# Optimization experiments

Measured on AMD Instinct MI355X. Metric: run time of the kernel, lower is better.

## Reference

```python
import jax, jax.numpy as jnp
import numpy as np

D_MODEL = 2048
D_STATE = 16
KER = 4
DT_RANK = D_MODEL // 16  # mamba default: ceil(d_model/16) = 128
B_SZ = 2
SEQ = 1024


def setup_inputs() -> dict:
    key = jax.random.key(0)
    ks = jax.random.split(key, 8)
    s = 0.02
    return {
        "x": jax.random.normal(ks[0], (B_SZ, SEQ, D_MODEL), jnp.float32),
        # in_proj: d_model -> 2*d_inner (expand=1 so d_inner=d_model)
        "W_in": jax.random.normal(ks[1], (2 * D_MODEL, D_MODEL), jnp.float32) * s,
        # depthwise causal conv, one kernel of length KER per channel
        "conv_w": jax.random.normal(ks[2], (D_MODEL, KER), jnp.float32) * s,
        "conv_b": jnp.zeros((D_MODEL,), jnp.float32),
        # x_proj: d_inner -> dt_rank + 2*d_state
        "W_xproj": jax.random.normal(ks[3], (DT_RANK + 2 * D_STATE, D_MODEL), jnp.float32) * s,
        # dt_proj: dt_rank -> d_inner
        "W_dt": jax.random.normal(ks[4], (D_MODEL, DT_RANK), jnp.float32) * s,
        "b_dt": jax.random.uniform(ks[5], (D_MODEL,), jnp.float32, -4.0, -2.0),
        # S4D-real init: A = -[1..d_state] per channel, stored as log
        "A_log": jnp.log(jnp.broadcast_to(jnp.arange(1, D_STATE + 1, dtype=jnp.float32), (D_MODEL, D_STATE))),
        "Dskip": jnp.ones((D_MODEL,), jnp.float32),
        # out_proj: d_inner -> d_model
        "W_out": jax.random.normal(ks[6], (D_MODEL, D_MODEL), jnp.float32) * s,
    }


def _mamba(x, W_in, conv_w, conv_b, W_xproj, W_dt, b_dt, A_log, Dskip, W_out):
    Bsz, L, dm = x.shape
    d_state = A_log.shape[1]
    dt_rank = W_dt.shape[1]
    K = conv_w.shape[1]

    # in_proj -> gate z and ssm input u
    xz = x @ W_in.T                      # [B, L, 2*d_inner]
    u, z = jnp.split(xz, 2, axis=-1)     # each [B, L, d_inner]

    # causal depthwise conv1d over time, then SiLU
    up = jnp.pad(u, ((0, 0), (K - 1, 0), (0, 0)))
    conv = conv_b + sum(conv_w[:, k] * up[:, k:k + L, :] for k in range(K))
    u = jax.nn.silu(conv)                # [B, L, d_inner]

    # input-dependent dt, B, C
    x_dbl = u @ W_xproj.T                # [B, L, dt_rank + 2*d_state]
    dt_r = x_dbl[..., :dt_rank]
    Bm = x_dbl[..., dt_rank:dt_rank + d_state]      # [B, L, N]
    Cm = x_dbl[..., dt_rank + d_state:]             # [B, L, N]
    dt = jax.nn.softplus(dt_r @ W_dt.T + b_dt)      # [B, L, d_inner]

    A = -jnp.exp(A_log)                             # [d_inner, N]
    dA = jnp.exp(dt[..., None] * A)                 # [B, L, d_inner, N]
    dBu = dt[..., None] * Bm[:, :, None, :] * u[..., None]  # [B, L, d_inner, N]

    def step(h, inp):
        dA_t, dBu_t, C_t = inp
        h = dA_t * h + dBu_t                        # [B, d_inner, N]
        y_t = jnp.einsum('bdn,bn->bd', h, C_t)      # [B, d_inner]
        return h, y_t

    h0 = jnp.zeros((Bsz, dm, d_state), dtype=x.dtype)
    _, ys = jax.lax.scan(step, h0,
                         (dA.swapaxes(0, 1), dBu.swapaxes(0, 1), Cm.swapaxes(0, 1)))
    y = ys.swapaxes(0, 1) + u * Dskip               # [B, L, d_inner]
    y = y * jax.nn.silu(z)
    return y @ W_out.T                              # [B, L, d_model]


def reference(x, W_in, conv_w, conv_b, W_xproj, W_dt, b_dt, A_log, Dskip, W_out):
    return _mamba(x, W_in, conv_w, conv_b, W_xproj, W_dt, b_dt, A_log, Dskip, W_out)
```

## Files before the change

### kernel.cpp

```cpp
#include <hip/hip_runtime.h>
#include <hip/hip_bf16.h>


#define D_MODEL 2048
#define D_STATE 16
#define KER 4
#define DT_RANK 128
#define B_SZ 2
#define SEQ 1024
#define BL (B_SZ * SEQ)
#define XPROJ_N (DT_RANK + 2 * D_STATE)
#define NC 32
#define TC (SEQ / NC)

using f32x4  = __attribute__((ext_vector_type(4))) float;
using bf16x8 = __attribute__((ext_vector_type(8))) __bf16;
using bf16x4 = __attribute__((ext_vector_type(4))) __bf16;

__device__ __forceinline__ float softplusf(float x) {
    return (x > 20.f) ? x : log1pf(__expf(x));
}
__device__ __forceinline__ float siluf(float x) {
    return x / (1.f + __expf(-x));
}

__global__ __launch_bounds__(256) void split_kernel(
    const float* __restrict__ src,
    __bf16* __restrict__ hi, __bf16* __restrict__ lo, int n4)
{
    int i = blockIdx.x * 256 + threadIdx.x;
    if (i >= n4) return;
    float4 v = *reinterpret_cast<const float4*>(&src[(size_t)i * 4]);
    bf16x4 hv, lv;
    float f[4] = {v.x, v.y, v.z, v.w};
    #pragma unroll
    for (int j = 0; j < 4; ++j) {
        __bf16 h = (__bf16)f[j];
        hv[j] = h;
        lv[j] = (__bf16)(f[j] - (float)h);
    }
    *reinterpret_cast<bf16x4*>(&hi[(size_t)i * 4]) = hv;
    *reinterpret_cast<bf16x4*>(&lo[(size_t)i * 4]) = lv;
}

__global__ __launch_bounds__(256, 2) void gemm_bf3(
    const __bf16* __restrict__ Ah, const __bf16* __restrict__ Al,
    const __bf16* __restrict__ Wh, const __bf16* __restrict__ Wl,
    float* __restrict__ C, int N_, int K)
{
    __shared__ __align__(16) __bf16 lds[4 * 128 * 64];
    __bf16* sAh = lds;
    __bf16* sAl = lds + 8192;
    __bf16* sWh = lds + 16384;
    __bf16* sWl = lds + 24576;

    const int tid = threadIdx.x;
    const int bm = blockIdx.y * 128;
    const int bn = blockIdx.x * 128;
    const int w  = tid >> 6;
    const int l  = tid & 63;
    const int wr = (w >> 1) * 64;
    const int wc = (w & 1) * 64;
    const int fr = l & 15;
    const int fq = l >> 4;

    f32x4 acc[4][4] = {};

    for (int k0 = 0; k0 < K; k0 += 64) {
        #pragma unroll
        for (int i = 0; i < 4; ++i) {
            const int f  = i * 256 + tid;
            const int r  = f >> 3;
            const int ss = f & 7;
            const int gs = ss ^ (r & 7);
            const size_t ga = (size_t)(bm + r) * K + k0 + gs * 8;
            const size_t gw = (size_t)(bn + r) * K + k0 + gs * 8;
            __builtin_amdgcn_global_load_lds(
                (const __attribute__((address_space(1))) void*)(Ah + ga),
                (__attribute__((address_space(3))) void*)(sAh + (size_t)f * 8), 16, 0, 0);
            __builtin_amdgcn_global_load_lds(
                (const __attribute__((address_space(1))) void*)(Al + ga),
                (__attribute__((address_space(3))) void*)(sAl + (size_t)f * 8), 16, 0, 0);
            __builtin_amdgcn_global_load_lds(
                (const __attribute__((address_space(1))) void*)(Wh + gw),
                (__attribute__((address_space(3))) void*)(sWh + (size_t)f * 8), 16, 0, 0);
            __builtin_amdgcn_global_load_lds(
                (const __attribute__((address_space(1))) void*)(Wl + gw),
                (__attribute__((address_space(3))) void*)(sWl + (size_t)f * 8), 16, 0, 0);
        }
        __syncthreads();

        #pragma unroll
        for (int ks = 0; ks < 2; ++ks) {
            bf16x8 ah[4], al[4], wh[4], wl[4];
            #pragma unroll
            for (int t = 0; t < 4; ++t) {
                const int ra = wr + t * 16 + fr;
                const int sa = (ks * 4 + fq) ^ (ra & 7);
                ah[t] = *reinterpret_cast<const bf16x8*>(&sAh[ra * 64 + sa * 8]);
                al[t] = *reinterpret_cast<const bf16x8*>(&sAl[ra * 64 + sa * 8]);
                const int rw = wc + t * 16 + fr;
                const int sw = (ks * 4 + fq) ^ (rw & 7);
                wh[t] = *reinterpret_cast<const bf16x8*>(&sWh[rw * 64 + sw * 8]);
                wl[t] = *reinterpret_cast<const bf16x8*>(&sWl[rw * 64 + sw * 8]);
            }
            #pragma unroll
            for (int mt = 0; mt < 4; ++mt)
                #pragma unroll
                for (int nt = 0; nt < 4; ++nt) {
                    acc[mt][nt] = __builtin_amdgcn_mfma_f32_16x16x32_bf16(
                        ah[mt], wh[nt], acc[mt][nt], 0, 0, 0);
                    acc[mt][nt] = __builtin_amdgcn_mfma_f32_16x16x32_bf16(
                        ah[mt], wl[nt], acc[mt][nt], 0, 0, 0);
                    acc[mt][nt] = __builtin_amdgcn_mfma_f32_16x16x32_bf16(
                        al[mt], wh[nt], acc[mt][nt], 0, 0, 0);
                }
        }
        __syncthreads();
    }

    #pragma unroll
    for (int mt = 0; mt < 4; ++mt)
        #pragma unroll
        for (int nt = 0; nt < 4; ++nt)
            #pragma unroll
            for (int j = 0; j < 4; ++j)
                C[(size_t)(bm + wr + mt * 16 + fq * 4 + j) * N_
                  + bn + wc + nt * 16 + fr] = acc[mt][nt][j];
}

#define BM 64
#define BN 64
#define BKT 32

template <int EPI>
__global__ __launch_bounds__(256) void gemm_nt(
    const float* __restrict__ A, int lda,
    const float* __restrict__ W, int ldw,
    float* __restrict__ C, int ldc,
    const float* __restrict__ bias,
    int M, int N, int K)
{
    __shared__ float As[BKT][BM + 4];
    __shared__ float Ws[BKT][BN + 4];

    const int tid = threadIdx.x;
    const int bm = blockIdx.y * BM;
    const int bn = blockIdx.x * BN;
    const int tx = tid & 15;
    const int ty = tid >> 4;

    float acc[4][4] = {};

    for (int k0 = 0; k0 < K; k0 += BKT) {
        #pragma unroll
        for (int i = 0; i < 2; ++i) {
            int f = tid + i * 256;
            int row = f >> 3;
            int kq  = f & 7;
            float4 v = *reinterpret_cast<const float4*>(
                &A[(size_t)(bm + row) * lda + k0 + kq * 4]);
            As[kq * 4 + 0][row] = v.x;
            As[kq * 4 + 1][row] = v.y;
            As[kq * 4 + 2][row] = v.z;
            As[kq * 4 + 3][row] = v.w;
        }
        #pragma unroll
        for (int i = 0; i < 2; ++i) {
            int f = tid + i * 256;
            int row = f >> 3;
            int kq  = f & 7;
            int gn = bn + row;
            float4 v = make_float4(0.f, 0.f, 0.f, 0.f);
            if (gn < N) {
                v = *reinterpret_cast<const float4*>(
                    &W[(size_t)gn * ldw + k0 + kq * 4]);
            }
            Ws[kq * 4 + 0][row] = v.x;
            Ws[kq * 4 + 1][row] = v.y;
            Ws[kq * 4 + 2][row] = v.z;
            Ws[kq * 4 + 3][row] = v.w;
        }
        __syncthreads();

        #pragma unroll
        for (int kk = 0; kk < BKT; ++kk) {
            float4 a4 = *reinterpret_cast<const float4*>(&As[kk][ty * 4]);
            float4 w4 = *reinterpret_cast<const float4*>(&Ws[kk][tx * 4]);
            float a[4] = {a4.x, a4.y, a4.z, a4.w};
            float wv[4] = {w4.x, w4.y, w4.z, w4.w};
            #pragma unroll
            for (int i = 0; i < 4; ++i)
                #pragma unroll
                for (int j = 0; j < 4; ++j)
                    acc[i][j] = fmaf(a[i], wv[j], acc[i][j]);
        }
        __syncthreads();
    }

    #pragma unroll
    for (int i = 0; i < 4; ++i) {
        int gm = bm + ty * 4 + i;
        #pragma unroll
        for (int j = 0; j < 4; ++j) {
            int gn = bn + tx * 4 + j;
            if (gn < N) {
                float v = acc[i][j];
                if (EPI == 1) v = softplusf(v + bias[gn]);
                C[(size_t)gm * ldc + gn] = v;
            }
        }
    }
}

#define XBM 64
#define XBN 32
#define XKS 8
#define XKC (D_MODEL / XKS)

__global__ __launch_bounds__(256) void xdbl_partial(
    const float* __restrict__ A,
    const float* __restrict__ W,
    float* __restrict__ P)
{
    __shared__ float As[BKT][XBM + 4];
    __shared__ float Ws[BKT][XBN + 4];

    const int tid = threadIdx.x;
    const int bm = blockIdx.y * XBM;
    const int bn = blockIdx.x * XBN;
    const int ks = blockIdx.z;
    const int tx = tid & 7;
    const int ty = tid >> 3;

    float acc[2][4] = {};

    const int kend = (ks + 1) * XKC;
    for (int k0 = ks * XKC; k0 < kend; k0 += BKT) {
        #pragma unroll
        for (int i = 0; i < 2; ++i) {
            int f = tid + i * 256;
            int row = f >> 3;
            int kq  = f & 7;
            float4 v = *reinterpret_cast<const float4*>(
                &A[(size_t)(bm + row) * D_MODEL + k0 + kq * 4]);
            As[kq * 4 + 0][row] = v.x;
            As[kq * 4 + 1][row] = v.y;
            As[kq * 4 + 2][row] = v.z;
            As[kq * 4 + 3][row] = v.w;
        }
        {
            int row = tid >> 3;
            int kq  = tid & 7;
            float4 v = *reinterpret_cast<const float4*>(
                &W[(size_t)(bn + row) * D_MODEL + k0 + kq * 4]);
            Ws[kq * 4 + 0][row] = v.x;
            Ws[kq * 4 + 1][row] = v.y;
            Ws[kq * 4 + 2][row] = v.z;
            Ws[kq * 4 + 3][row] = v.w;
        }
        __syncthreads();

        #pragma unroll
        for (int kk = 0; kk < BKT; ++kk) {
            float a0 = As[kk][ty * 2 + 0];
            float a1 = As[kk][ty * 2 + 1];
            float4 w4 = *reinterpret_cast<const float4*>(&Ws[kk][tx * 4]);
            float wv[4] = {w4.x, w4.y, w4.z, w4.w};
            #pragma unroll
            for (int j = 0; j < 4; ++j) {
                acc[0][j] = fmaf(a0, wv[j], acc[0][j]);
                acc[1][j] = fmaf(a1, wv[j], acc[1][j]);
            }
        }
        __syncthreads();
    }

    #pragma unroll
    for (int i = 0; i < 2; ++i) {
        const int gm = bm + ty * 2 + i;
        #pragma unroll
        for (int j = 0; j < 4; ++j) {
            const int gn = bn + tx * 4 + j;
            P[((size_t)ks * BL + gm) * XPROJ_N + gn] = acc[i][j];
        }
    }
}

__global__ __launch_bounds__(256) void xdbl_reduce(
    const float* __restrict__ P, float* __restrict__ xdbl)
{
    const int i = blockIdx.x * 256 + threadIdx.x;
    const int n4 = BL * XPROJ_N / 4;
    if (i >= n4) return;
    float4 s = *reinterpret_cast<const float4*>(&P[(size_t)i * 4]);
    #pragma unroll
    for (int ks = 1; ks < XKS; ++ks) {
        float4 v = *reinterpret_cast<const float4*>(
            &P[(size_t)ks * BL * XPROJ_N + (size_t)i * 4]);
        s.x += v.x; s.y += v.y; s.z += v.z; s.w += v.w;
    }
    *reinterpret_cast<float4*>(&xdbl[(size_t)i * 4]) = s;
}

__global__ __launch_bounds__(256) void conv_silu_kernel(
    const float* __restrict__ xz,
    const float* __restrict__ conv_w,
    const float* __restrict__ conv_b,
    float* __restrict__ u)
{
    int idx = blockIdx.x * blockDim.x + threadIdx.x;
    if (idx >= BL * D_MODEL) return;
    int d  = idx & (D_MODEL - 1);
    int bl = idx >> 11;
    int l  = bl & (SEQ - 1);
    int b  = bl >> 10;

    float acc = conv_b[d];
    #pragma unroll
    for (int k = 0; k < KER; ++k) {
        int ls = l - (KER - 1) + k;
        if (ls >= 0) {
            acc = fmaf(conv_w[d * KER + k],
                       xz[(size_t)(b * SEQ + ls) * (2 * D_MODEL) + d], acc);
        }
    }
    u[(size_t)idx] = siluf(acc);
}

__global__ __launch_bounds__(256) void scan_part1(
    const float* __restrict__ dt,
    const float* __restrict__ xdbl,
    const float* __restrict__ u,
    const float* __restrict__ A_log,
    float* __restrict__ PH,
    float* __restrict__ Hend)
{
    const int tid = threadIdx.x;
    const int d   = blockIdx.x * 256 + tid;
    const int bc  = blockIdx.y;
    const int b   = bc >> 5;
    const int c   = bc & (NC - 1);

    float A[16];
    #pragma unroll
    for (int q = 0; q < 4; ++q) {
        float4 v = *reinterpret_cast<const float4*>(&A_log[d * 16 + q * 4]);
        A[q*4+0] = -__expf(v.x); A[q*4+1] = -__expf(v.y);
        A[q*4+2] = -__expf(v.z); A[q*4+3] = -__expf(v.w);
    }
    float h[16] = {};
    float P[16];
    #pragma unroll
    for (int n = 0; n < 16; ++n) P[n] = 1.f;

    const size_t row0 = (size_t)b * SEQ + c * TC;
    for (int t = 0; t < TC; ++t) {
        const size_t row = row0 + t;
        const float dtv = dt[row * D_MODEL + d];
        const float uv  = u[row * D_MODEL + d];
        float Bv[16];
        const float4* Bp = reinterpret_cast<const float4*>(&xdbl[row * XPROJ_N + DT_RANK]);
        #pragma unroll
        for (int q = 0; q < 4; ++q) {
            float4 v = Bp[q];
            Bv[q*4+0] = v.x; Bv[q*4+1] = v.y; Bv[q*4+2] = v.z; Bv[q*4+3] = v.w;
        }
        const float dtu = dtv * uv;
        #pragma unroll
        for (int n = 0; n < 16; ++n) {
            float dA = __expf(dtv * A[n]);
            h[n] = fmaf(dA, h[n], dtu * Bv[n]);
            P[n] *= dA;
        }
    }
    const size_t off = ((size_t)bc * D_MODEL + d) * 16;
    #pragma unroll
    for (int q = 0; q < 4; ++q) {
        *reinterpret_cast<float4*>(&PH[off + q*4])   =
            make_float4(P[q*4+0], P[q*4+1], P[q*4+2], P[q*4+3]);
        *reinterpret_cast<float4*>(&Hend[off + q*4]) =
            make_float4(h[q*4+0], h[q*4+1], h[q*4+2], h[q*4+3]);
    }
}

__global__ __launch_bounds__(256) void scan_part2(
    float* __restrict__ PH,
    const float* __restrict__ Hend)
{
    const int g  = blockIdx.x * 256 + threadIdx.x;
    const int b  = g >> 15;
    const int dn = g & 32767;
    float h = 0.f;
    #pragma unroll
    for (int c = 0; c < NC; ++c) {
        const size_t off = ((size_t)(b * NC + c) * D_MODEL * 16) + dn;
        const float p  = PH[off];
        const float he = Hend[off];
        PH[off] = h;
        h = fmaf(p, h, he);
    }
}

__global__ __launch_bounds__(256) void scan_part3(
    const float* __restrict__ dt,
    const float* __restrict__ xdbl,
    const float* __restrict__ xz,
    const float* __restrict__ u,
    const float* __restrict__ A_log,
    const float* __restrict__ Dskip,
    const float* __restrict__ PH,
    float* __restrict__ yact)
{
    const int tid = threadIdx.x;
    const int d   = blockIdx.x * 256 + tid;
    const int bc  = blockIdx.y;
    const int b   = bc >> 5;
    const int c   = bc & (NC - 1);

    float A[16];
    #pragma unroll
    for (int q = 0; q < 4; ++q) {
        float4 v = *reinterpret_cast<const float4*>(&A_log[d * 16 + q * 4]);
        A[q*4+0] = -__expf(v.x); A[q*4+1] = -__expf(v.y);
        A[q*4+2] = -__expf(v.z); A[q*4+3] = -__expf(v.w);
    }
    float h[16];
    const size_t off = ((size_t)bc * D_MODEL + d) * 16;
    #pragma unroll
    for (int q = 0; q < 4; ++q) {
        float4 v = *reinterpret_cast<const float4*>(&PH[off + q*4]);
        h[q*4+0] = v.x; h[q*4+1] = v.y; h[q*4+2] = v.z; h[q*4+3] = v.w;
    }
    const float Dk = Dskip[d];

    const size_t row0 = (size_t)b * SEQ + c * TC;
    for (int t = 0; t < TC; ++t) {
        const size_t row = row0 + t;
        const float dtv = dt[row * D_MODEL + d];
        const float uv  = u[row * D_MODEL + d];
        float Bv[16], Cv[16];
        const float4* Bp = reinterpret_cast<const float4*>(&xdbl[row * XPROJ_N + DT_RANK]);
        const float4* Cp = reinterpret_cast<const float4*>(&xdbl[row * XPROJ_N + DT_RANK + D_STATE]);
        #pragma unroll
        for (int q = 0; q < 4; ++q) {
            float4 v = Bp[q];
            Bv[q*4+0] = v.x; Bv[q*4+1] = v.y; Bv[q*4+2] = v.z; Bv[q*4+3] = v.w;
            float4 wv = Cp[q];
            Cv[q*4+0] = wv.x; Cv[q*4+1] = wv.y; Cv[q*4+2] = wv.z; Cv[q*4+3] = wv.w;
        }
        const float dtu = dtv * uv;
        float y = 0.f;
        #pragma unroll
        for (int n = 0; n < 16; ++n) {
            float dA = __expf(dtv * A[n]);
            h[n] = fmaf(dA, h[n], dtu * Bv[n]);
            y = fmaf(h[n], Cv[n], y);
        }
        const float zv = xz[row * (2 * D_MODEL) + D_MODEL + d];
        const float yv = y + uv * Dk;
        yact[row * D_MODEL + d] = yv * siluf(zv);
    }
}

extern "C" void kernel_launch(void* const* d_in, const int* in_sizes, int n_in,
                              void* d_out, int out_size, void* d_ws, size_t ws_size,
                              hipStream_t stream) {
    const float* x       = (const float*)d_in[0];
    const float* W_in    = (const float*)d_in[1];
    const float* conv_w  = (const float*)d_in[2];
    const float* conv_b  = (const float*)d_in[3];
    const float* W_xproj = (const float*)d_in[4];
    const float* W_dt    = (const float*)d_in[5];
    const float* b_dt    = (const float*)d_in[6];
    const float* A_log   = (const float*)d_in[7];
    const float* Dskip   = (const float*)d_in[8];
    const float* W_out   = (const float*)d_in[9];
    float* out = (float*)d_out;

    float* ws = (float*)d_ws;
    const size_t M1 = 1024 * 1024;
    float* xz   = ws;
    float* u    = ws + 8 * M1;
    float* xdbl = ws + 12 * M1;
    float* dt   = ws + 12 * M1 + 512 * 1024;
    float* yact = dt + 4 * M1;
    float* PH   = yact + 4 * M1;
    float* Hend = PH + 2 * M1;

    __bf16* planes = (__bf16*)(ws + 25 * M1);
    __bf16* xh  = planes;
    __bf16* xl  = xh + 4 * M1;
    __bf16* wih = xl + 4 * M1;
    __bf16* wil = wih + 8 * M1;
    __bf16* woh = wih;
    __bf16* wol = wih + 4 * M1;
    __bf16* yh  = xh;
    __bf16* yl  = xl;
    float* xpart = (float*)(ws + 25 * M1);

    split_kernel<<<(BL * D_MODEL / 4 + 255) / 256, 256, 0, stream>>>(x, xh, xl, BL * D_MODEL / 4);
    split_kernel<<<(2 * D_MODEL * D_MODEL / 4 + 255) / 256, 256, 0, stream>>>(
        W_in, wih, wil, 2 * D_MODEL * D_MODEL / 4);

    {
        dim3 grid(2 * D_MODEL / 128, BL / 128);
        gemm_bf3<<<grid, 256, 0, stream>>>(xh, xl, wih, wil, xz, 2 * D_MODEL, D_MODEL);
    }
    conv_silu_kernel<<<BL * D_MODEL / 256, 256, 0, stream>>>(xz, conv_w, conv_b, u);

    split_kernel<<<(D_MODEL * D_MODEL / 4 + 255) / 256, 256, 0, stream>>>(
        W_out, woh, wol, D_MODEL * D_MODEL / 4);

    {
        dim3 grid(XPROJ_N / XBN, BL / XBM, XKS);
        xdbl_partial<<<grid, 256, 0, stream>>>(u, W_xproj, xpart);
        xdbl_reduce<<<(BL * XPROJ_N / 4 + 255) / 256, 256, 0, stream>>>(xpart, xdbl);
    }
    {
        dim3 grid(D_MODEL / BN, BL / BM);
        gemm_nt<1><<<grid, 256, 0, stream>>>(xdbl, XPROJ_N, W_dt, DT_RANK,
                                             dt, D_MODEL, b_dt,
                                             BL, D_MODEL, DT_RANK);
    }
    {
        dim3 grid(D_MODEL / 256, B_SZ * NC);
        scan_part1<<<grid, 256, 0, stream>>>(dt, xdbl, u, A_log, PH, Hend);
        scan_part2<<<B_SZ * D_MODEL * 16 / 256, 256, 0, stream>>>(PH, Hend);
        scan_part3<<<grid, 256, 0, stream>>>(dt, xdbl, xz, u, A_log, Dskip, PH, yact);
    }
    split_kernel<<<(BL * D_MODEL / 4 + 255) / 256, 256, 0, stream>>>(yact, yh, yl, BL * D_MODEL / 4);

    {
        dim3 grid(D_MODEL / 128, BL / 128);
        gemm_bf3<<<grid, 256, 0, stream>>>(yh, yl, woh, wol, out, D_MODEL, D_MODEL);
    }
}
```

Measured before the change: 430.0 us.

## Double-buffer bf16x3 GEMM LDS tiles and fuse y split into scan

The bf16x3 GEMM now uses a BK=32 double-buffered LDS layout, issuing the global-to-LDS loads for the next k-tile before computing the current one, with a new 4-slot XOR swizzle. The scan's final kernel writes the hi/lo bf16 planes of the gated output directly, which removes the separate split kernel and the fp32 yact round trip. The smaller k-tile means more loop iterations and barriers, and with only one barrier per iteration the overlap relies on load ordering.

```diff
diff --git a/kernel.cpp b/kernel.cpp
--- a/kernel.cpp
+++ b/kernel.cpp
@@ -48,11 +48,7 @@
     const __bf16* __restrict__ Wh, const __bf16* __restrict__ Wl,
     float* __restrict__ C, int N_, int K)
 {
-    __shared__ __align__(16) __bf16 lds[4 * 128 * 64];
-    __bf16* sAh = lds;
-    __bf16* sAl = lds + 8192;
-    __bf16* sWh = lds + 16384;
-    __bf16* sWl = lds + 24576;
+    __shared__ __align__(16) __bf16 lds[2 * 4 * 128 * 32];
 
     const int tid = threadIdx.x;
     const int bm = blockIdx.y * 128;
@@ -66,56 +62,62 @@
 
     f32x4 acc[4][4] = {};
 
-    for (int k0 = 0; k0 < K; k0 += 64) {
-        #pragma unroll
-        for (int i = 0; i < 4; ++i) {
+    auto stage = [&](int buf, int k0) {
+        __bf16* base = lds + buf * 16384;
+        #pragma unroll
+        for (int i = 0; i < 2; ++i) {
             const int f  = i * 256 + tid;
-            const int r  = f >> 3;
-            const int ss = f & 7;
-            const int gs = ss ^ (r & 7);
+            const int r  = f >> 2;
+            const int gs = (f & 3) ^ ((r >> 1) & 3);
             const size_t ga = (size_t)(bm + r) * K + k0 + gs * 8;
             const size_t gw = (size_t)(bn + r) * K + k0 + gs * 8;
             __builtin_amdgcn_global_load_lds(
                 (const __attribute__((address_space(1))) void*)(Ah + ga),
-                (__attribute__((address_space(3))) void*)(sAh + (size_t)f * 8), 16, 0, 0);
+                (__attribute__((address_space(3))) void*)(base + (size_t)f * 8), 16, 0, 0);
             __builtin_amdgcn_global_load_lds(
                 (const __attribute__((address_space(1))) void*)(Al + ga),
-                (__attribute__((address_space(3))) void*)(sAl + (size_t)f * 8), 16, 0, 0);
+                (__attribute__((address_space(3))) void*)(base + 4096 + (size_t)f * 8), 16, 0, 0);
             __builtin_amdgcn_global_load_lds(
                 (const __attribute__((address_space(1))) void*)(Wh + gw),
-                (__attribute__((address_space(3))) void*)(sWh + (size_t)f * 8), 16, 0, 0);
+                (__attribute__((address_space(3))) void*)(base + 8192 + (size_t)f * 8), 16, 0, 0);
             __builtin_amdgcn_global_load_lds(
                 (const __attribute__((address_space(1))) void*)(Wl + gw),
-                (__attribute__((address_space(3))) void*)(sWl + (size_t)f * 8), 16, 0, 0);
-        }
-        __syncthreads();
-
-        #pragma unroll
-        for (int ks = 0; ks < 2; ++ks) {
-            bf16x8 ah[4], al[4], wh[4], wl[4];
+                (__attribute__((address_space(3))) void*)(base + 12288 + (size_t)f * 8), 16, 0, 0);
+        }
+    };
+
+    stage(0, 0);
+    __syncthreads();
+
+    const int NT = K / 32;
+    for (int kt = 0; kt < NT; ++kt) {
+        const int cur = kt & 1;
+        if (kt + 1 < NT) stage(cur ^ 1, (kt + 1) * 32);
+
+        const __bf16* base = lds + cur * 16384;
+        bf16x8 ah[4], al[4], wh[4], wl[4];
+        #pragma unroll
+        for (int t = 0; t < 4; ++t) {
+            const int ra = wr + t * 16 + fr;
+            const int sa = fq ^ ((ra >> 1) & 3);
+            ah[t] = *reinterpret_cast<const bf16x8*>(base + ra * 32 + sa * 8);
+            al[t] = *reinterpret_cast<const bf16x8*>(base + 4096 + ra * 32 + sa * 8);
+            const int rw = wc + t * 16 + fr;
+            const int sw = fq ^ ((rw >> 1) & 3);
+            wh[t] = *reinterpret_cast<const bf16x8*>(base + 8192 + rw * 32 + sw * 8);
+            wl[t] = *reinterpret_cast<const bf16x8*>(base + 12288 + rw * 32 + sw * 8);
+        }
+        #pragma unroll
+        for (int mt = 0; mt < 4; ++mt)
             #pragma unroll
-            for (int t = 0; t < 4; ++t) {
-                const int ra = wr + t * 16 + fr;
-                const int sa = (ks * 4 + fq) ^ (ra & 7);
-                ah[t] = *reinterpret_cast<const bf16x8*>(&sAh[ra * 64 + sa * 8]);
-                al[t] = *reinterpret_cast<const bf16x8*>(&sAl[ra * 64 + sa * 8]);
-                const int rw = wc + t * 16 + fr;
-                const int sw = (ks * 4 + fq) ^ (rw & 7);
-                wh[t] = *reinterpret_cast<const bf16x8*>(&sWh[rw * 64 + sw * 8]);
-                wl[t] = *reinterpret_cast<const bf16x8*>(&sWl[rw * 64 + sw * 8]);
+            for (int nt = 0; nt < 4; ++nt) {
+                acc[mt][nt] = __builtin_amdgcn_mfma_f32_16x16x32_bf16(
+                    ah[mt], wh[nt], acc[mt][nt], 0, 0, 0);
+                acc[mt][nt] = __builtin_amdgcn_mfma_f32_16x16x32_bf16(
+                    ah[mt], wl[nt], acc[mt][nt], 0, 0, 0);
+                acc[mt][nt] = __builtin_amdgcn_mfma_f32_16x16x32_bf16(
+                    al[mt], wh[nt], acc[mt][nt], 0, 0, 0);
             }
-            #pragma unroll
-            for (int mt = 0; mt < 4; ++mt)
-                #pragma unroll
-                for (int nt = 0; nt < 4; ++nt) {
-                    acc[mt][nt] = __builtin_amdgcn_mfma_f32_16x16x32_bf16(
-                        ah[mt], wh[nt], acc[mt][nt], 0, 0, 0);
-                    acc[mt][nt] = __builtin_amdgcn_mfma_f32_16x16x32_bf16(
-                        ah[mt], wl[nt], acc[mt][nt], 0, 0, 0);
-                    acc[mt][nt] = __builtin_amdgcn_mfma_f32_16x16x32_bf16(
-                        al[mt], wh[nt], acc[mt][nt], 0, 0, 0);
-                }
-        }
         __syncthreads();
     }
 
@@ -410,7 +412,7 @@
     const float* __restrict__ A_log,
     const float* __restrict__ Dskip,
     const float* __restrict__ PH,
-    float* __restrict__ yact)
+    __bf16* __restrict__ yh, __bf16* __restrict__ yl)
 {
     const int tid = threadIdx.x;
     const int d   = blockIdx.x * 256 + tid;
@@ -458,8 +460,10 @@
             y = fmaf(h[n], Cv[n], y);
         }
         const float zv = xz[row * (2 * D_MODEL) + D_MODEL + d];
-        const float yv = y + uv * Dk;
-        yact[row * D_MODEL + d] = yv * siluf(zv);
+        const float yv = (y + uv * Dk) * siluf(zv);
+        const __bf16 hv = (__bf16)yv;
+        yh[row * D_MODEL + d] = hv;
+        yl[row * D_MODEL + d] = (__bf16)(yv - (float)hv);
     }
 }
 
@@ -484,8 +488,7 @@
     float* u    = ws + 8 * M1;
     float* xdbl = ws + 12 * M1;
     float* dt   = ws + 12 * M1 + 512 * 1024;
-    float* yact = dt + 4 * M1;
-    float* PH   = yact + 4 * M1;
+    float* PH   = dt + 4 * M1;
     float* Hend = PH + 2 * M1;
 
     __bf16* planes = (__bf16*)(ws + 25 * M1);
@@ -527,10 +530,8 @@
         dim3 grid(D_MODEL / 256, B_SZ * NC);
         scan_part1<<<grid, 256, 0, stream>>>(dt, xdbl, u, A_log, PH, Hend);
         scan_part2<<<B_SZ * D_MODEL * 16 / 256, 256, 0, stream>>>(PH, Hend);
-        scan_part3<<<grid, 256, 0, stream>>>(dt, xdbl, xz, u, A_log, Dskip, PH, yact);
-    }
-    split_kernel<<<(BL * D_MODEL / 4 + 255) / 256, 256, 0, stream>>>(yact, yh, yl, BL * D_MODEL / 4);
-
+        scan_part3<<<grid, 256, 0, stream>>>(dt, xdbl, xz, u, A_log, Dskip, PH, yh, yl);
+    }
     {
         dim3 grid(D_MODEL / 128, BL / 128);
         gemm_bf3<<<grid, 256, 0, stream>>>(yh, yl, woh, wol, out, D_MODEL, D_MODEL);
```

Result: no change. 429.4 us (-0.1%).
